# Performance work log

Measured on AMD Instinct MI355X. Metric: run time of the kernel, lower is better.

Reference implementation:

```python
import jax, jax.numpy as jnp
import numpy as np

S, B, V, E, H = 64, 32, 32000, 512, 1024


def gru_cell(x, h, Wih, Whh, bih, bhh):
    # PyTorch GRU cell math. x: [B, in], h: [B, H]
    gi = x @ Wih.T + bih          # [B, 3H]
    gh = h @ Whh.T + bhh          # [B, 3H]
    ir, iz, inn = jnp.split(gi, 3, axis=-1)
    hr, hz, hn = jnp.split(gh, 3, axis=-1)
    r = jax.nn.sigmoid(ir + hr)
    z = jax.nn.sigmoid(iz + hz)
    n = jnp.tanh(inn + r * hn)
    return (1.0 - z) * n + z * h


def run_gru(xs, h0, Wih, Whh, bih, bhh):
    def step(h, x):
        h = gru_cell(x, h, Wih, Whh, bih, bhh)
        return h, h
    _, hs = jax.lax.scan(step, h0, xs)
    return hs  # [S, B, H]


def setup_inputs():
    key = jax.random.key(0)
    ks = jax.random.split(key, 24)
    n = lambda k, shp, s=0.05: (jax.random.normal(k, shp, jnp.float32) * s)
    inp = {
        "input_seq": jax.random.randint(ks[0], (S, B), 0, V),
        "target_seq": jax.random.randint(ks[1], (S, B), 0, V),
        "emb": n(ks[2], (V, E)),
        # bidirectional encoder GRU (forward / backward directions)
        "enc_Wih_f": n(ks[3], (3 * H, E)), "enc_Whh_f": n(ks[4], (3 * H, H)),
        "enc_bih_f": n(ks[5], (3 * H,)),  "enc_bhh_f": n(ks[6], (3 * H,)),
        "enc_Wih_b": n(ks[7], (3 * H, E)), "enc_Whh_b": n(ks[8], (3 * H, H)),
        "enc_bih_b": n(ks[9], (3 * H,)),  "enc_bhh_b": n(ks[10], (3 * H,)),
        "encoder_init": n(ks[11], (2, H), 0.1),
        # decoder GRU: input = token(E) + glimpse(2H) + last_output(E)
        "dec_Wih": n(ks[12], (3 * H, 2 * E + 2 * H)), "dec_Whh": n(ks[13], (3 * H, H)),
        "dec_bih": n(ks[14], (3 * H,)), "dec_bhh": n(ks[15], (3 * H,)),
        "dec_init_h": n(ks[16], (H,), 0.1),
        "dec_init_out": n(ks[17], (E,), 0.1),
        "attn_W1": n(ks[18], (H, 3 * H)),  # Linear(3H -> H, bias=False)
        "attn_W2": n(ks[19], (1, H)),      # Linear(H -> 1, bias=False)
        "out_W": n(ks[20], (V, H)), "out_b": n(ks[21], (V,)),
    }
    return inp


def reference(input_seq, target_seq, emb,
              enc_Wih_f, enc_Whh_f, enc_bih_f, enc_bhh_f,
              enc_Wih_b, enc_Whh_b, enc_bih_b, enc_bhh_b, encoder_init,
              dec_Wih, dec_Whh, dec_bih, dec_bhh, dec_init_h, dec_init_out,
              attn_W1, attn_W2, out_W, out_b):
    x = emb[input_seq]            # [S, B, E]
    tgt = emb[target_seq]         # [S, B, E]
    bsz = x.shape[1]

    # bidirectional encoder
    h0f = jnp.broadcast_to(encoder_init[0], (bsz, H))
    h0b = jnp.broadcast_to(encoder_init[1], (bsz, H))
    fwd = run_gru(x, h0f, enc_Wih_f, enc_Whh_f, enc_bih_f, enc_bhh_f)
    bwd = run_gru(x[::-1], h0b, enc_Wih_b, enc_Whh_b, enc_bih_b, enc_bhh_b)[::-1]
    enc = jnp.concatenate([fwd, bwd], axis=-1)  # [S, B, 2H]

    def step(carry, inp_t):
        h, last_out = carry                      # [B,H], [B,E]
        tok, tg = inp_t                          # [B,E], [B,E]
        hexp = jnp.broadcast_to(h[None], (S, bsz, H))
        a = jnp.concatenate([enc, hexp], axis=-1)            # [S, B, 3H]
        scores = jnp.tanh(a @ attn_W1.T) @ attn_W2.T          # [S, B, 1]
        # NOTE: original uses nn.Softmax(dim=1) on [S,B,1] -> softmax over BATCH dim
        w = jax.nn.softmax(scores, axis=1)
        glimpse = (enc * w).sum(axis=0)                       # [B, 2H]
        dec_in = jnp.concatenate([tok, glimpse, last_out], axis=-1)
        h = gru_cell(dec_in, h, dec_Wih, dec_Whh, dec_bih, dec_bhh)
        probs = jax.nn.softmax(h @ out_W.T + out_b, axis=1)   # [B, V]
        return (h, tg), probs

    h0 = jnp.broadcast_to(dec_init_h, (bsz, H))
    o0 = jnp.broadcast_to(dec_init_out, (bsz, E))
    _, outs = jax.lax.scan(step, (h0, o0), (x, tgt))
    return outs  # [S, B, V]
```

## Files before the change

### kernel.cpp

```cpp
#include <hip/hip_runtime.h>
#include <hip/hip_bf16.h>

#define S_ 64
#define B_ 32
#define V_ 32000
#define E_ 512
#define H_ 1024
#define H3_ 3072

typedef __hip_bfloat16 bf16;
typedef __attribute__((ext_vector_type(8))) short s8v;
typedef __attribute__((ext_vector_type(4))) float f4;
typedef unsigned long long ull;

__device__ __forceinline__ float b2f(bf16 x){ return __bfloat162float(x); }
__device__ __forceinline__ bf16  f2b(float x){ return __float2bfloat16(x); }
__device__ __forceinline__ float bfu2f(unsigned short u){
  union { unsigned u; float f; } c; c.u = ((unsigned)u) << 16; return c.f;
}
#define MFMA16(a,b,c) __builtin_amdgcn_mfma_f32_16x16x32_bf16((a),(b),(c),0,0,0)

__device__ __forceinline__ float fsigmoid(float x){ return 1.f/(1.f + __expf(-x)); }
__device__ __forceinline__ float ftanh(float x){ float e2 = __expf(2.f*x); return 1.f - 2.f/(e2 + 1.f); }

__global__ __launch_bounds__(256) void cast_bf16_k(const float* __restrict__ s, bf16* __restrict__ d, int n8){
  int stride = gridDim.x*256;
  for (int i = blockIdx.x*256 + threadIdx.x; i < n8; i += stride){
    f4 a = *((const f4*)s + (size_t)i*2);
    f4 b = *((const f4*)s + (size_t)i*2 + 1);
    union { s8v v; bf16 h[8]; } o;
    #pragma unroll
    for (int k=0;k<4;k++){ o.h[k]=f2b(a[k]); o.h[4+k]=f2b(b[k]); }
    *((s8v*)d + i) = o.v;
  }
}
__global__ __launch_bounds__(256) void cast2_k(const float* __restrict__ s0, const float* __restrict__ s1,
                                               bf16* __restrict__ d0, bf16* __restrict__ d1, int n8){
  const float* s = blockIdx.y ? s1 : s0;
  bf16* d = blockIdx.y ? d1 : d0;
  int stride = gridDim.x*256;
  for (int i = blockIdx.x*256 + threadIdx.x; i < n8; i += stride){
    f4 a = *((const f4*)s + (size_t)i*2);
    f4 b = *((const f4*)s + (size_t)i*2 + 1);
    union { s8v v; bf16 h[8]; } o;
    #pragma unroll
    for (int k=0;k<4;k++){ o.h[k]=f2b(a[k]); o.h[4+k]=f2b(b[k]); }
    *((s8v*)d + i) = o.v;
  }
}
__global__ __launch_bounds__(256) void cast4_k(const float* __restrict__ s0, const float* __restrict__ s1,
                                               const float* __restrict__ s2, const float* __restrict__ s3,
                                               bf16* __restrict__ d0, bf16* __restrict__ d1,
                                               bf16* __restrict__ d2, bf16* __restrict__ d3, int n8){
  const float* s = (blockIdx.y==0)?s0:(blockIdx.y==1)?s1:(blockIdx.y==2)?s2:s3;
  bf16* d = (blockIdx.y==0)?d0:(blockIdx.y==1)?d1:(blockIdx.y==2)?d2:d3;
  int stride = gridDim.x*256;
  for (int i = blockIdx.x*256 + threadIdx.x; i < n8; i += stride){
    f4 a = *((const f4*)s + (size_t)i*2);
    f4 b = *((const f4*)s + (size_t)i*2 + 1);
    union { s8v v; bf16 h[8]; } o;
    #pragma unroll
    for (int k=0;k<4;k++){ o.h[k]=f2b(a[k]); o.h[4+k]=f2b(b[k]); }
    *((s8v*)d + i) = o.v;
  }
}
__global__ __launch_bounds__(256) void gather2_k(const float* __restrict__ emb,
                                                 const int* __restrict__ iseq, const int* __restrict__ tseq,
                                                 const float* __restrict__ o0,
                                                 bf16* __restrict__ dx, bf16* __restrict__ dlo){
  int i = blockIdx.x*256 + threadIdx.x;
  int row = i >> 6, e8 = i & 63;
  const float* src;
  bf16* d;
  if (blockIdx.y == 0){
    src = emb + (size_t)iseq[row]*E_;
    d = dx;
  } else {
    int t = row >> 5, b = row & 31;
    src = (t == 0) ? o0 : (emb + (size_t)tseq[(t-1)*B_ + b]*E_);
    d = dlo;
  }
  f4 a = *((const f4*)src + e8*2);
  f4 b = *((const f4*)src + e8*2 + 1);
  union { s8v v; bf16 h[8]; } o;
  #pragma unroll
  for (int k=0;k<4;k++){ o.h[k]=f2b(a[k]); o.h[4+k]=f2b(b[k]); }
  *((s8v*)d + i) = o.v;
}

template<int WB16, int ACC>
__global__ __launch_bounds__(256) void gemm_bt(const bf16* __restrict__ A, int lda,
                                               const bf16* __restrict__ B, int ldb,
                                               const float* __restrict__ bias,
                                               void* __restrict__ Cp, int ldc, int K)
{
  __shared__ bf16 a_sm[128][40];
  __shared__ bf16 b_sm[128][40];
  const int tid = threadIdx.x;
  const int m0 = blockIdx.y*128, n0 = blockIdx.x*128;
  const int w = tid>>6, l = tid&63;
  const int wm = w>>1, wn = w&1;
  f4 acc[4][4];
  #pragma unroll
  for (int i=0;i<4;i++)
    #pragma unroll
    for (int j=0;j<4;j++) acc[i][j] = (f4){0.f,0.f,0.f,0.f};
  const int srow = tid>>1, skc = (tid&1)*16;
  const int ar = l&15, koff = (l>>4)*8;
  for (int k0 = 0; k0 < K; k0 += 32){
    __syncthreads();
    const s8v* pa = (const s8v*)(A + (size_t)(m0+srow)*lda + k0 + skc);
    const s8v* pb = (const s8v*)(B + (size_t)(n0+srow)*ldb + k0 + skc);
    *(s8v*)&a_sm[srow][skc]   = pa[0];
    *(s8v*)&a_sm[srow][skc+8] = pa[1];
    *(s8v*)&b_sm[srow][skc]   = pb[0];
    *(s8v*)&b_sm[srow][skc+8] = pb[1];
    __syncthreads();
    s8v av[4], bv[4];
    #pragma unroll
    for (int i=0;i<4;i++) av[i] = *(const s8v*)&a_sm[wm*64 + i*16 + ar][koff];
    #pragma unroll
    for (int j=0;j<4;j++) bv[j] = *(const s8v*)&b_sm[wn*64 + j*16 + ar][koff];
    #pragma unroll
    for (int i=0;i<4;i++)
      #pragma unroll
      for (int j=0;j<4;j++)
        acc[i][j] = MFMA16(av[i], bv[j], acc[i][j]);
  }
  const int rb = (l>>4)*4;
  #pragma unroll
  for (int i=0;i<4;i++){
    #pragma unroll
    for (int j=0;j<4;j++){
      int col = n0 + wn*64 + j*16 + ar;
      float badd = bias ? bias[col] : 0.f;
      #pragma unroll
      for (int r=0;r<4;r++){
        int row = m0 + wm*64 + i*16 + rb + r;
        size_t idx = (size_t)row*ldc + col;
        float v = acc[i][j][r] + badd;
        if (ACC) v += ((const float*)Cp)[idx];
        if (WB16) ((bf16*)Cp)[idx] = f2b(v);
        else      ((float*)Cp)[idx] = v;
      }
    }
  }
}

__global__ __launch_bounds__(256) void out_gemm_k(
  const bf16* __restrict__ A, const bf16* __restrict__ Bw,
  const float* __restrict__ bias, bf16* __restrict__ C)
{
  __shared__ bf16 a_sm[128][40];
  __shared__ bf16 b_sm[128][40];
  const int tid = threadIdx.x;
  const int bid = blockIdx.x;
  const int xcd = bid & 7, kk = bid >> 3;
  const int super = kk >> 6, rem = kk & 63;
  const int sm = super & 1, sn = super >> 1;
  const int mi = rem & 7, nj = rem >> 3;
  const int mt = sm*8 + mi, nl = sn*8 + nj;
  const int nt = nl*8 + xcd;
  if (nt >= 250) return;
  const int m0 = mt*128, n0 = nt*128;
  const int w = tid>>6, l = tid&63;
  const int wm = w>>1, wn = w&1;
  f4 acc[4][4];
  #pragma unroll
  for (int i=0;i<4;i++)
    #pragma unroll
    for (int j=0;j<4;j++) acc[i][j] = (f4){0.f,0.f,0.f,0.f};
  const int srow = tid>>1, skc = (tid&1)*16;
  const int ar = l&15, koff = (l>>4)*8;
  for (int k0 = 0; k0 < 1024; k0 += 32){
    __syncthreads();
    const s8v* pa = (const s8v*)(A + (size_t)(m0+srow)*1024 + k0 + skc);
    const s8v* pb = (const s8v*)(Bw + (size_t)(n0+srow)*1024 + k0 + skc);
    *(s8v*)&a_sm[srow][skc]   = pa[0];
    *(s8v*)&a_sm[srow][skc+8] = pa[1];
    *(s8v*)&b_sm[srow][skc]   = pb[0];
    *(s8v*)&b_sm[srow][skc+8] = pb[1];
    __syncthreads();
    s8v av[4], bv[4];
    #pragma unroll
    for (int i=0;i<4;i++) av[i] = *(const s8v*)&a_sm[wm*64 + i*16 + ar][koff];
    #pragma unroll
    for (int j=0;j<4;j++) bv[j] = *(const s8v*)&b_sm[wn*64 + j*16 + ar][koff];
    #pragma unroll
    for (int i=0;i<4;i++)
      #pragma unroll
      for (int j=0;j<4;j++)
        acc[i][j] = MFMA16(av[i], bv[j], acc[i][j]);
  }
  const int rb = (l>>4)*4;
  float bj[4];
  #pragma unroll
  for (int j=0;j<4;j++) bj[j] = bias[n0 + wn*64 + j*16 + ar];
  #pragma unroll
  for (int i=0;i<4;i++){
    #pragma unroll
    for (int j=0;j<4;j++){
      const int col = n0 + wn*64 + j*16 + ar;
      #pragma unroll
      for (int r=0;r<4;r++){
        const int row = m0 + wm*64 + i*16 + rb + r;
        C[(size_t)row*V_ + col] = f2b(acc[i][j][r] + bj[j]);
      }
    }
  }
}

__global__ __launch_bounds__(256) void logit_stats_k(const bf16* __restrict__ lg,
                                                     float* __restrict__ rowM, float* __restrict__ rowL){
  __shared__ float wm[4], wl[4];
  const int tid = threadIdx.x;
  const bf16* p = lg + (size_t)blockIdx.x*V_;
  float m = -1e30f, lsum = 0.f;
  for (int c = tid; c < V_/8; c += 256){
    union { s8v v; unsigned short us[8]; } u;
    u.v = *((const s8v*)p + c);
    #pragma unroll
    for (int k = 0; k < 8; ++k){
      float v = bfu2f(u.us[k]);
      float mn = fmaxf(m, v);
      lsum = lsum*__expf(m - mn) + __expf(v - mn);
      m = mn;
    }
  }
  #pragma unroll
  for (int o = 32; o; o >>= 1){
    float mo = __shfl_xor(m, o), lo_ = __shfl_xor(lsum, o);
    float mn = fmaxf(m, mo);
    lsum = lsum*__expf(m - mn) + lo_*__expf(mo - mn);
    m = mn;
  }
  if ((tid&63)==0){ wm[tid>>6] = m; wl[tid>>6] = lsum; }
  __syncthreads();
  if (tid == 0){
    float M = fmaxf(fmaxf(wm[0],wm[1]), fmaxf(wm[2],wm[3]));
    float L = wl[0]*__expf(wm[0]-M) + wl[1]*__expf(wm[1]-M)
            + wl[2]*__expf(wm[2]-M) + wl[3]*__expf(wm[3]-M);
    rowM[blockIdx.x] = M;
    rowL[blockIdx.x] = L;
  }
}

__global__ __launch_bounds__(256) void norm_k(const bf16* __restrict__ lg,
                                              const float* __restrict__ rowM, const float* __restrict__ rowL,
                                              float* __restrict__ out){
  const int tid = threadIdx.x;
  const int row = blockIdx.x;
  const float M = rowM[row], inv = 1.f/rowL[row];
  const bf16* p = lg + (size_t)row*V_;
  float* q = out + (size_t)row*V_;
  for (int c = tid; c < V_/8; c += 256){
    union { s8v v; unsigned short us[8]; } u;
    u.v = *((const s8v*)p + c);
    f4 o0, o1;
    #pragma unroll
    for (int k = 0; k < 4; ++k) o0[k] = __expf(bfu2f(u.us[k]) - M)*inv;
    #pragma unroll
    for (int k = 0; k < 4; ++k) o1[k] = __expf(bfu2f(u.us[4+k]) - M)*inv;
    *((f4*)q + c*2)     = o0;
    *((f4*)q + c*2 + 1) = o1;
  }
}

__global__ __launch_bounds__(256) void enc_init_k(const float* __restrict__ enc_init,
                                                  const float* __restrict__ bihf, const float* __restrict__ bihb,
                                                  bf16* __restrict__ hb0, float* __restrict__ hfE,
                                                  float* __restrict__ bias_fb){
  int i = blockIdx.x*256 + threadIdx.x;
  int base = i*8;
  int dir = base>>15, rem = base&32767, col = rem&1023;
  const float* sp = enc_init + dir*H_ + col;
  f4 a = *(const f4*)sp, b = *(const f4*)(sp+4);
  union { s8v v; bf16 h[8]; } o;
  #pragma unroll
  for (int k=0;k<4;k++){ o.h[k]=f2b(a[k]); o.h[4+k]=f2b(b[k]); }
  *(s8v*)(hb0 + dir*32768 + rem) = o.v;
  *(f4*)(hfE + dir*32768 + rem) = a;
  *(f4*)(hfE + dir*32768 + rem + 4) = b;
  if (i < 6144) bias_fb[i] = (i < 3072) ? bihf[i] : bihb[i-3072];
}
__global__ __launch_bounds__(256) void dec_init_k(const float* __restrict__ dinh,
                                                  bf16* __restrict__ hd0, float* __restrict__ hfD){
  int i = blockIdx.x*256 + threadIdx.x;
  int base = i*8;
  int col = base&1023;
  const float* sp = dinh + col;
  f4 a = *(const f4*)sp, b = *(const f4*)(sp+4);
  union { s8v v; bf16 h[8]; } o;
  #pragma unroll
  for (int k=0;k<4;k++){ o.h[k]=f2b(a[k]); o.h[4+k]=f2b(b[k]); }
  *(s8v*)(hd0 + base) = o.v;
  *(f4*)(hfD + base) = a;
  *(f4*)(hfD + base + 4) = b;
}

__global__ __launch_bounds__(256) void enc_step_k(
  const float* __restrict__ gi_fb,
  const bf16* __restrict__ whhf, const bf16* __restrict__ whhb,
  const float* __restrict__ bhhf, const float* __restrict__ bhhb,
  const bf16* __restrict__ hrd_base, bf16* __restrict__ hwr_base,
  float* __restrict__ hfE, bf16* __restrict__ enc_out, int s)
{
  __shared__ bf16 hst[16][1032];
  __shared__ bf16 hsT[16][64];
  const int tid = threadIdx.x, bid = blockIdx.x;
  const int w = tid>>6, l = tid&63;
  const int lr = l&15, koff = (l>>4)*8, rb = (l>>4)*4;
  const int x = bid&7, g3 = bid>>3;
  const int dir = x>>2;
  const int mt = g3>>2;
  const int jtb = (x&3)*16 + (g3&3)*4;
  const int jt = jtb + w;
  const int col = jt*16 + lr;
  const bf16* W    = dir ? whhb : whhf;
  const float* bhh = dir ? bhhb : bhhf;
  const float br_ = bhh[col], bz_ = bhh[H_+col], bn_ = bhh[2*H_+col];
  const bf16* pr = W + (size_t)(jt*16 + lr)*H_ + koff;
  const bf16* pz = pr + (size_t)H_*H_;
  const bf16* pn = pz + (size_t)H_*H_;
  {
    const bf16* src = hrd_base + dir*32768 + (size_t)mt*16*H_;
    #pragma unroll
    for (int c = 0; c < 8; ++c){
      int g = c*256 + tid;
      int row = g>>7, off = g&127;
      *(s8v*)&hst[row][off*8] = *(const s8v*)(src + (size_t)row*H_ + off*8);
    }
  }
  __syncthreads();
  f4 accr = (f4){0,0,0,0}, accz = (f4){0,0,0,0}, accn = (f4){0,0,0,0};
  #pragma unroll 4
  for (int k0 = 0; k0 < H_; k0 += 32){
    s8v a = *(const s8v*)&hst[lr][koff + k0];
    accr = MFMA16(a, *(const s8v*)(pr + k0), accr);
    accz = MFMA16(a, *(const s8v*)(pz + k0), accz);
    accn = MFMA16(a, *(const s8v*)(pn + k0), accn);
  }
  const int es = dir ? (63 - s) : s;
  const int dcol = dir*3072 + col;
  #pragma unroll
  for (int ri = 0; ri < 4; ++ri){
    const int b_ = mt*16 + rb + ri;
    const size_t gr = (size_t)(es*B_ + b_)*6144;
    float ir = gi_fb[gr + dcol], iz = gi_fb[gr + 1024 + dcol], inn = gi_fb[gr + 2048 + dcol];
    float rg = fsigmoid(ir + accr[ri] + br_);
    float zg = fsigmoid(iz + accz[ri] + bz_);
    float ng = ftanh(inn + rg*(accn[ri] + bn_));
    float hold = hfE[dir*32768 + b_*H_ + col];
    float hnew = (1.f - zg)*ng + zg*hold;
    hfE[dir*32768 + b_*H_ + col] = hnew;
    hsT[rb+ri][w*16+lr] = f2b(hnew);
  }
  __syncthreads();
  {
    const int row = tid>>4, seg = tid&15;
    ull v = *(ull*)&hsT[row][seg*4];
    *(ull*)(hwr_base + dir*32768 + (size_t)(mt*16+row)*H_ + jtb*16 + seg*4) = v;
    *(ull*)(enc_out + (size_t)(es*B_ + mt*16+row)*2048 + dir*H_ + jtb*16 + seg*4) = v;
  }
}

__global__ __launch_bounds__(256) void dec_k1(
  const bf16* __restrict__ hd,
  const bf16* __restrict__ whhd, const float* __restrict__ bhhd,
  const bf16* __restrict__ w1b,
  float* __restrict__ gh, bf16* __restrict__ hW1b)
{
  __shared__ bf16 hst[16][1032];
  __shared__ float ghT[16][128];
  __shared__ bf16 hwT[16][128];
  const int tid = threadIdx.x, bid = blockIdx.x;
  const int w = tid>>6, l = tid&63;
  const int lr = l&15, koff = (l>>4)*8;
  const bool isP = bid < 16;
  const int hmt = isP ? (bid&1) : ((bid-16)&1);
  {
    const bf16* src = hd + (size_t)hmt*16*H_;
    #pragma unroll
    for (int c = 0; c < 8; ++c){
      int g = c*256 + tid;
      int row = g>>7, off = g&127;
      *(s8v*)&hst[row][off*8] = *(const s8v*)(src + (size_t)row*H_ + off*8);
    }
  }
  __syncthreads();
  if (isP){
    const int x2 = bid>>1;
    const int pjt0 = x2*8 + w*2;
    #pragma unroll
    for (int q = 0; q < 2; ++q){
      const bf16* pb = w1b + (size_t)((pjt0+q)*16 + lr)*H3_ + 2048 + koff;
      f4 acc = (f4){0,0,0,0};
      #pragma unroll 4
      for (int k0 = 0; k0 < H_; k0 += 32)
        acc = MFMA16(*(const s8v*)&hst[lr][koff+k0], *(const s8v*)(pb+k0), acc);
      #pragma unroll
      for (int r = 0; r < 4; ++r)
        hwT[(l>>4)*4+r][(w*2+q)*16 + lr] = f2b(acc[r]);
    }
    __syncthreads();
    #pragma unroll
    for (int i = 0; i < 2; ++i){
      int idx = tid + i*256;
      int row = idx>>5, seg = idx&31;
      *(ull*)(hW1b + (size_t)(hmt*16+row)*H_ + x2*128 + seg*4) = *(ull*)&hwT[row][seg*4];
    }
  } else {
    const int gb = bid - 16;
    const int rest = gb>>1;
    const int x3 = rest/3, gkk = rest%3;
    const int ntb = x3*24 + gkk*8;
    #pragma unroll
    for (int q = 0; q < 2; ++q){
      const int nt = ntb + w*2 + q;
      const bf16* pb = whhd + (size_t)(nt*16 + lr)*H_ + koff;
      const float bv = bhhd[nt*16 + lr];
      f4 acc = (f4){0,0,0,0};
      #pragma unroll 4
      for (int k0 = 0; k0 < H_; k0 += 32)
        acc = MFMA16(*(const s8v*)&hst[lr][koff+k0], *(const s8v*)(pb+k0), acc);
      #pragma unroll
      for (int r = 0; r < 4; ++r)
        ghT[(l>>4)*4+r][(w*2+q)*16 + lr] = acc[r] + bv;
    }
    __syncthreads();
    #pragma unroll
    for (int i = 0; i < 4; ++i){
      int idx = tid + i*256;
      int row = idx>>6, seg = idx&63;
      union{ float f[2]; ull u; } pk;
      pk.f[0] = ghT[row][seg*2]; pk.f[1] = ghT[row][seg*2+1];
      *(ull*)(gh + (size_t)(hmt*16+row)*H3_ + ntb*16 + seg*2) = pk.u;
    }
  }
}

__global__ __launch_bounds__(256) void dec_k2(
  const bf16* __restrict__ encW1b, const bf16* __restrict__ hW1b,
  const float* __restrict__ attnW2, float* __restrict__ wat)
{
  __shared__ float w2st[1024];
  __shared__ float scl[32];
  const int tid = threadIdx.x, s = blockIdx.x;
  w2st[tid] = attnW2[tid];
  w2st[tid+256] = attnW2[tid+256];
  w2st[tid+512] = attnW2[tid+512];
  w2st[tid+768] = attnW2[tid+768];
  __syncthreads();
  const int b = tid>>3, part = tid&7;
  const bf16* hp = hW1b + (size_t)b*H_ + part*128;
  const bf16* ep = encW1b + ((size_t)s*B_ + b)*H_ + part*128;
  const float* wp = w2st + part*128;
  float p = 0.f;
  #pragma unroll 4
  for (int ii = 0; ii < 16; ++ii){
    union { s8v v; unsigned short uu[8]; } hv, ev;
    hv.v = *(const s8v*)(hp + ii*8);
    ev.v = *(const s8v*)(ep + ii*8);
    #pragma unroll
    for (int k = 0; k < 8; ++k){
      float xx = bfu2f(ev.uu[k]) + bfu2f(hv.uu[k]);
      p += wp[ii*8+k]*ftanh(xx);
    }
  }
  p += __shfl_xor(p,1); p += __shfl_xor(p,2); p += __shfl_xor(p,4);
  if (part == 0) scl[b] = p;
  __syncthreads();
  if (tid < 32){
    float v = scl[tid];
    float m = v;
    #pragma unroll
    for (int o = 1; o <= 16; o <<= 1) m = fmaxf(m, __shfl_xor(m, o));
    float e = __expf(v - m);
    float Z = e;
    #pragma unroll
    for (int o = 1; o <= 16; o <<= 1) Z += __shfl_xor(Z, o);
    wat[s*B_ + tid] = e/Z;
  }
}

__global__ __launch_bounds__(256) void dec_k3(
  const float* __restrict__ gi_t,
  const bf16* __restrict__ encWgb, const float* __restrict__ gh,
  const float* __restrict__ wat,
  float* __restrict__ hfD, bf16* __restrict__ hd_w, bf16* __restrict__ hall_t)
{
  __shared__ float watst[64];
  __shared__ float part_[4][3][256];
  __shared__ bf16 hnewst[256];
  const int tid = threadIdx.x, bid = blockIdx.x;
  const int x = bid&7, g3 = bid>>3;
  const int db = 4*x + (g3&3), jq = g3>>2;
  const int jD = jq*256 + tid;
  if (tid < 64) watst[tid] = wat[tid*B_ + db];
  __syncthreads();
  const int lane = tid&63, wv = tid>>6;
  const int j0 = jq*256 + lane*4;
  f4 g0 = (f4){0,0,0,0}, g1 = (f4){0,0,0,0}, g2 = (f4){0,0,0,0};
  #pragma unroll 4
  for (int i = 0; i < 16; ++i){
    const int s2 = wv*16 + i;
    const float wt = watst[s2];
    const bf16* ro = encWgb + ((size_t)s2*B_ + db)*H3_;
    union{ ull u; unsigned short us[4]; } v0, v1, v2;
    v0.u = *(const ull*)(ro + j0);
    v1.u = *(const ull*)(ro + H_ + j0);
    v2.u = *(const ull*)(ro + 2*H_ + j0);
    #pragma unroll
    for (int k = 0; k < 4; ++k){
      g0[k] += wt*bfu2f(v0.us[k]);
      g1[k] += wt*bfu2f(v1.us[k]);
      g2[k] += wt*bfu2f(v2.us[k]);
    }
  }
  *(f4*)&part_[wv][0][lane*4] = g0;
  *(f4*)&part_[wv][1][lane*4] = g1;
  *(f4*)&part_[wv][2][lane*4] = g2;
  __syncthreads();
  float G0 = part_[0][0][tid]+part_[1][0][tid]+part_[2][0][tid]+part_[3][0][tid];
  float G1 = part_[0][1][tid]+part_[1][1][tid]+part_[2][1][tid]+part_[3][1][tid];
  float G2 = part_[0][2][tid]+part_[1][2][tid]+part_[2][2][tid]+part_[3][2][tid];
  const float* gp = gi_t + (size_t)db*H3_ + jD;
  float ir  = gp[0]    + G0;
  float iz  = gp[H_]   + G1;
  float inn = gp[2*H_] + G2;
  float hr_ = gh[(size_t)db*H3_ + jD];
  float hz_ = gh[(size_t)db*H3_ + H_ + jD];
  float hn_ = gh[(size_t)db*H3_ + 2*H_ + jD];
  float rg = fsigmoid(ir + hr_);
  float zg = fsigmoid(iz + hz_);
  float ng = ftanh(inn + rg*hn_);
  float hold = hfD[(size_t)db*H_ + jD];
  float hnew = (1.f - zg)*ng + zg*hold;
  hfD[(size_t)db*H_ + jD] = hnew;
  hnewst[tid] = f2b(hnew);
  __syncthreads();
  if (tid < 64){
    ull v = *(ull*)&hnewst[tid*4];
    *(ull*)(hd_w + (size_t)db*H_ + jq*256 + tid*4) = v;
    *(ull*)(hall_t + (size_t)db*H_ + jq*256 + tid*4) = v;
  }
}

extern "C" void kernel_launch(void* const* d_in, const int* in_sizes, int n_in,
                              void* d_out, int out_size, void* d_ws, size_t ws_size,
                              hipStream_t stream)
{
  (void)in_sizes; (void)n_in; (void)out_size; (void)ws_size;
  const int*   iseq  = (const int*)d_in[0];
  const int*   tseq  = (const int*)d_in[1];
  const float* emb   = (const float*)d_in[2];
  const float* wihf  = (const float*)d_in[3];
  const float* whhf_f= (const float*)d_in[4];
  const float* bihf  = (const float*)d_in[5];
  const float* bhhf  = (const float*)d_in[6];
  const float* wihb  = (const float*)d_in[7];
  const float* whhb_f= (const float*)d_in[8];
  const float* bihb  = (const float*)d_in[9];
  const float* bhhb  = (const float*)d_in[10];
  const float* einit = (const float*)d_in[11];
  const float* wihd  = (const float*)d_in[12];
  const float* whhd_f= (const float*)d_in[13];
  const float* bihd  = (const float*)d_in[14];
  const float* bhhd  = (const float*)d_in[15];
  const float* dinh  = (const float*)d_in[16];
  const float* dino  = (const float*)d_in[17];
  const float* w1    = (const float*)d_in[18];
  const float* w2    = (const float*)d_in[19];
  const float* outw  = (const float*)d_in[20];
  const float* outb  = (const float*)d_in[21];
  float* out = (float*)d_out;

  char* ws = (char*)d_ws;
  size_t off = 0;
  auto alloc = [&](size_t bytes)->char*{ char* p = ws + off; off += (bytes + 255) & ~(size_t)255; return p; };
  bf16* logits_b = (bf16*)ws;
  bf16* x_b      = (bf16*)alloc((size_t)2048*512*2);
  bf16* lo_b     = (bf16*)alloc((size_t)2048*512*2);
  bf16* wihf_b   = (bf16*)alloc((size_t)3072*512*2);
  bf16* wihb_b   = (bf16*)alloc((size_t)3072*512*2);
  bf16* whhf_b   = (bf16*)alloc((size_t)3072*1024*2);
  bf16* whhb_b   = (bf16*)alloc((size_t)3072*1024*2);
  bf16* wihd_b   = (bf16*)alloc((size_t)3072*3072*2);
  bf16* whhd_b   = (bf16*)alloc((size_t)3072*1024*2);
  bf16* w1_b     = (bf16*)alloc((size_t)1024*3072*2);
  float* gi_fb   = (float*)alloc((size_t)2048*6144*4);
  float* gi_d    = (float*)alloc((size_t)2048*3072*4);
  bf16* enc_b    = (bf16*)alloc((size_t)2048*2048*2);
  bf16* encW1_b  = (bf16*)alloc((size_t)2048*1024*2);
  bf16* encWg_b  = (bf16*)alloc((size_t)2048*3072*2);
  float* bias_fb = (float*)alloc((size_t)6144*4);
  bf16*  henc_b  = (bf16*)alloc((size_t)2*65536*2);
  float* hfE     = (float*)alloc((size_t)2*32768*4);
  bf16*  hdb     = (bf16*)alloc((size_t)2*32768*2);
  float* hfD     = (float*)alloc((size_t)32768*4);
  bf16*  hW1b    = (bf16*)alloc((size_t)32768*2);
  float* ghb     = (float*)alloc((size_t)32*3072*4);
  float* wat     = (float*)alloc((size_t)64*32*4);
  float* rowM    = (float*)alloc((size_t)2048*4);
  float* rowL    = (float*)alloc((size_t)2048*4);
  bf16* outw_b   = (bf16*)alloc((size_t)32000*1024*2);
  bf16*  hall_b  = (bf16*)alloc((size_t)2048*1024*2);

  gather2_k<<<dim3(512,2), 256, 0, stream>>>(emb, iseq, tseq, dino, x_b, lo_b);
  cast2_k<<<dim3(768,2),  256, 0, stream>>>(wihf, wihb, wihf_b, wihb_b, 196608);
  cast4_k<<<dim3(768,4),  256, 0, stream>>>(whhf_f, whhb_f, whhd_f, w1,
                                            whhf_b, whhb_b, whhd_b, w1_b, 393216);
  cast_bf16_k<<<2048, 256, 0, stream>>>(wihd, wihd_b, 1179648);
  cast_bf16_k<<<2048, 256, 0, stream>>>(outw, outw_b, 4096000);
  enc_init_k<<<32, 256, 0, stream>>>(einit, bihf, bihb, henc_b, hfE, bias_fb);

  gemm_bt<0,0><<<dim3(48,16), 256, 0, stream>>>(x_b, 512, wihf_b,      512,  bias_fb, gi_fb, 6144, 512);
  gemm_bt<0,0><<<dim3(24,16), 256, 0, stream>>>(x_b, 512, wihd_b,      3072, bihd,    gi_d,  3072, 512);
  gemm_bt<0,1><<<dim3(24,16), 256, 0, stream>>>(lo_b,512, wihd_b+2560, 3072, nullptr, gi_d,  3072, 512);

  for (int s = 0; s < 64; ++s){
    const bf16* hrd = henc_b + (size_t)(s&1)*65536;
    bf16*       hwr = henc_b + (size_t)((s+1)&1)*65536;
    enc_step_k<<<64, 256, 0, stream>>>(gi_fb, whhf_b, whhb_b, bhhf, bhhb,
                                       hrd, hwr, hfE, enc_b, s);
  }

  gemm_bt<1,0><<<dim3(8,16),  256, 0, stream>>>(enc_b, 2048, w1_b,       3072, nullptr, encW1_b, 1024, 2048);
  gemm_bt<1,0><<<dim3(24,16), 256, 0, stream>>>(enc_b, 2048, wihd_b+512, 3072, nullptr, encWg_b, 3072, 2048);

  dec_init_k<<<16, 256, 0, stream>>>(dinh, hdb, hfD);
  for (int t = 0; t < 64; ++t){
    const bf16* hdr = hdb + (size_t)(t&1)*32768;
    bf16*       hdw = hdb + (size_t)((t+1)&1)*32768;
    dec_k1<<<64, 256, 0, stream>>>(hdr, whhd_b, bhhd, w1_b, ghb, hW1b);
    dec_k2<<<64, 256, 0, stream>>>(encW1_b, hW1b, w2, wat);
    dec_k3<<<128, 256, 0, stream>>>(gi_d + (size_t)t*B_*H3_, encWg_b, ghb, wat,
                                    hfD, hdw, hall_b + (size_t)t*B_*H_);
  }

  out_gemm_k<<<4096, 256, 0, stream>>>(hall_b, outw_b, outb, logits_b);
  logit_stats_k<<<2048, 256, 0, stream>>>(logits_b, rowM, rowL);
  norm_k<<<2048, 256, 0, stream>>>(logits_b, rowM, rowL, out);
}
```

Measured before the change: 3.162 ms.

## Merge prep kernels, fuse decoder input GEMMs, use direct global-to-LDS loads

All weight casts, embedding gathers and state initialisations are folded into one multi-task prep kernel, which removes several launches. The two decoder input-projection GEMMs are merged into a single dual-A kernel, so the float accumulate read-modify-write pass goes away. The GEMM tiles now load through global_load_lds with an unpadded 32-column LDS layout, which may bring back LDS bank conflicts on the MFMA fragment reads. The prep kernel uses a fixed 512-block grid per task, so the large out_W cast loops more times per thread.

Result: faster. 3.083 ms (median of 2 runs) (-2.5%).

```diff
diff --git a/kernel.cpp b/kernel.cpp
--- a/kernel.cpp
+++ b/kernel.cpp
@@ -23,79 +23,108 @@
 __device__ __forceinline__ float fsigmoid(float x){ return 1.f/(1.f + __expf(-x)); }
 __device__ __forceinline__ float ftanh(float x){ float e2 = __expf(2.f*x); return 1.f - 2.f/(e2 + 1.f); }
 
-__global__ __launch_bounds__(256) void cast_bf16_k(const float* __restrict__ s, bf16* __restrict__ d, int n8){
-  int stride = gridDim.x*256;
-  for (int i = blockIdx.x*256 + threadIdx.x; i < n8; i += stride){
-    f4 a = *((const f4*)s + (size_t)i*2);
-    f4 b = *((const f4*)s + (size_t)i*2 + 1);
-    union { s8v v; bf16 h[8]; } o;
-    #pragma unroll
-    for (int k=0;k<4;k++){ o.h[k]=f2b(a[k]); o.h[4+k]=f2b(b[k]); }
-    *((s8v*)d + i) = o.v;
-  }
-}
-__global__ __launch_bounds__(256) void cast2_k(const float* __restrict__ s0, const float* __restrict__ s1,
-                                               bf16* __restrict__ d0, bf16* __restrict__ d1, int n8){
-  const float* s = blockIdx.y ? s1 : s0;
-  bf16* d = blockIdx.y ? d1 : d0;
-  int stride = gridDim.x*256;
-  for (int i = blockIdx.x*256 + threadIdx.x; i < n8; i += stride){
-    f4 a = *((const f4*)s + (size_t)i*2);
-    f4 b = *((const f4*)s + (size_t)i*2 + 1);
-    union { s8v v; bf16 h[8]; } o;
-    #pragma unroll
-    for (int k=0;k<4;k++){ o.h[k]=f2b(a[k]); o.h[4+k]=f2b(b[k]); }
-    *((s8v*)d + i) = o.v;
-  }
-}
-__global__ __launch_bounds__(256) void cast4_k(const float* __restrict__ s0, const float* __restrict__ s1,
-                                               const float* __restrict__ s2, const float* __restrict__ s3,
-                                               bf16* __restrict__ d0, bf16* __restrict__ d1,
-                                               bf16* __restrict__ d2, bf16* __restrict__ d3, int n8){
-  const float* s = (blockIdx.y==0)?s0:(blockIdx.y==1)?s1:(blockIdx.y==2)?s2:s3;
-  bf16* d = (blockIdx.y==0)?d0:(blockIdx.y==1)?d1:(blockIdx.y==2)?d2:d3;
-  int stride = gridDim.x*256;
-  for (int i = blockIdx.x*256 + threadIdx.x; i < n8; i += stride){
-    f4 a = *((const f4*)s + (size_t)i*2);
-    f4 b = *((const f4*)s + (size_t)i*2 + 1);
-    union { s8v v; bf16 h[8]; } o;
-    #pragma unroll
-    for (int k=0;k<4;k++){ o.h[k]=f2b(a[k]); o.h[4+k]=f2b(b[k]); }
-    *((s8v*)d + i) = o.v;
-  }
-}
-__global__ __launch_bounds__(256) void gather2_k(const float* __restrict__ emb,
-                                                 const int* __restrict__ iseq, const int* __restrict__ tseq,
-                                                 const float* __restrict__ o0,
-                                                 bf16* __restrict__ dx, bf16* __restrict__ dlo){
-  int i = blockIdx.x*256 + threadIdx.x;
-  int row = i >> 6, e8 = i & 63;
-  const float* src;
-  bf16* d;
-  if (blockIdx.y == 0){
-    src = emb + (size_t)iseq[row]*E_;
-    d = dx;
-  } else {
-    int t = row >> 5, b = row & 31;
-    src = (t == 0) ? o0 : (emb + (size_t)tseq[(t-1)*B_ + b]*E_);
-    d = dlo;
-  }
-  f4 a = *((const f4*)src + e8*2);
-  f4 b = *((const f4*)src + e8*2 + 1);
+__device__ __forceinline__ void gl16(const bf16* g, bf16* l){
+  __builtin_amdgcn_global_load_lds((const __attribute__((address_space(1))) void*)g,
+                                   (__attribute__((address_space(3))) void*)l, 16, 0, 0);
+}
+
+__device__ __forceinline__ void cast8(const float* __restrict__ s, bf16* __restrict__ d, int i){
+  f4 a = *((const f4*)s + (size_t)i*2);
+  f4 b = *((const f4*)s + (size_t)i*2 + 1);
   union { s8v v; bf16 h[8]; } o;
   #pragma unroll
   for (int k=0;k<4;k++){ o.h[k]=f2b(a[k]); o.h[4+k]=f2b(b[k]); }
   *((s8v*)d + i) = o.v;
 }
 
-template<int WB16, int ACC>
+__global__ __launch_bounds__(256) void prep_all_k(
+  const float* __restrict__ emb, const int* __restrict__ iseq, const int* __restrict__ tseq,
+  const float* __restrict__ dino,
+  const float* __restrict__ wihf, const float* __restrict__ wihb,
+  const float* __restrict__ whhf, const float* __restrict__ whhb,
+  const float* __restrict__ whhd, const float* __restrict__ w1,
+  const float* __restrict__ wihd, const float* __restrict__ outw,
+  const float* __restrict__ einit, const float* __restrict__ bihf,
+  const float* __restrict__ bihb, const float* __restrict__ dinh,
+  bf16* __restrict__ x_b, bf16* __restrict__ lo_b,
+  bf16* __restrict__ wihf_b, bf16* __restrict__ wihb_b,
+  bf16* __restrict__ whhf_b, bf16* __restrict__ whhb_b,
+  bf16* __restrict__ whhd_b, bf16* __restrict__ w1_b,
+  bf16* __restrict__ wihd_b, bf16* __restrict__ outw_b,
+  bf16* __restrict__ henc_b, float* __restrict__ hfE, float* __restrict__ bias_fb,
+  bf16* __restrict__ hdb, float* __restrict__ hfD)
+{
+  const int task = blockIdx.y;
+  const int stride = gridDim.x*256;
+  const int i00 = blockIdx.x*256 + threadIdx.x;
+  if (task < 8){
+    const float* s; bf16* d; int n8;
+    switch(task){
+      case 0: s=wihf; d=wihf_b; n8=196608; break;
+      case 1: s=wihb; d=wihb_b; n8=196608; break;
+      case 2: s=whhf; d=whhf_b; n8=393216; break;
+      case 3: s=whhb; d=whhb_b; n8=393216; break;
+      case 4: s=whhd; d=whhd_b; n8=393216; break;
+      case 5: s=w1;   d=w1_b;   n8=393216; break;
+      case 6: s=wihd; d=wihd_b; n8=1179648; break;
+      default: s=outw; d=outw_b; n8=4096000; break;
+    }
+    for (int i = i00; i < n8; i += stride) cast8(s, d, i);
+  } else if (task == 8 || task == 9){
+    for (int i = i00; i < 131072; i += stride){
+      int row = i>>6, e8 = i&63;
+      const float* src; bf16* d;
+      if (task == 8){ src = emb + (size_t)iseq[row]*E_; d = x_b; }
+      else {
+        int t = row>>5, b = row&31;
+        src = (t == 0) ? dino : (emb + (size_t)tseq[(t-1)*B_ + b]*E_);
+        d = lo_b;
+      }
+      f4 a = *((const f4*)src + e8*2);
+      f4 b = *((const f4*)src + e8*2 + 1);
+      union { s8v v; bf16 h[8]; } o;
+      #pragma unroll
+      for (int k=0;k<4;k++){ o.h[k]=f2b(a[k]); o.h[4+k]=f2b(b[k]); }
+      *((s8v*)d + i) = o.v;
+    }
+  } else if (task == 10){
+    for (int i = i00; i < 8192; i += stride){
+      int base = i*8;
+      int dir = base>>15, rem = base&32767, col = rem&1023;
+      const float* sp = einit + dir*H_ + col;
+      f4 a = *(const f4*)sp, b = *(const f4*)(sp+4);
+      union { s8v v; bf16 h[8]; } o;
+      #pragma unroll
+      for (int k=0;k<4;k++){ o.h[k]=f2b(a[k]); o.h[4+k]=f2b(b[k]); }
+      *(s8v*)(henc_b + dir*32768 + rem) = o.v;
+      *(f4*)(hfE + dir*32768 + rem) = a;
+      *(f4*)(hfE + dir*32768 + rem + 4) = b;
+      if (i < 6144) bias_fb[i] = (i < 3072) ? bihf[i] : bihb[i-3072];
+    }
+  } else {
+    for (int i = i00; i < 4096; i += stride){
+      int base = i*8;
+      int col = base&1023;
+      const float* sp = dinh + col;
+      f4 a = *(const f4*)sp, b = *(const f4*)(sp+4);
+      union { s8v v; bf16 h[8]; } o;
+      #pragma unroll
+      for (int k=0;k<4;k++){ o.h[k]=f2b(a[k]); o.h[4+k]=f2b(b[k]); }
+      *(s8v*)(hdb + base) = o.v;
+      *(f4*)(hfD + base) = a;
+      *(f4*)(hfD + base + 4) = b;
+    }
+  }
+}
+
+template<int WB16>
 __global__ __launch_bounds__(256) void gemm_bt(const bf16* __restrict__ A, int lda,
                                                const bf16* __restrict__ B, int ldb,
                                                const float* __restrict__ bias,
                                                void* __restrict__ Cp, int ldc, int K)
 {
-  __shared__ bf16 a_sm[128][40];
-  __shared__ bf16 b_sm[128][40];
+  __shared__ bf16 a_sm[128][32];
+  __shared__ bf16 b_sm[128][32];
   const int tid = threadIdx.x;
   const int m0 = blockIdx.y*128, n0 = blockIdx.x*128;
   const int w = tid>>6, l = tid&63;
@@ -105,16 +134,16 @@
   for (int i=0;i<4;i++)
     #pragma unroll
     for (int j=0;j<4;j++) acc[i][j] = (f4){0.f,0.f,0.f,0.f};
-  const int srow = tid>>1, skc = (tid&1)*16;
   const int ar = l&15, koff = (l>>4)*8;
+  const int glr = l>>2, gls = (l&3)*8;
   for (int k0 = 0; k0 < K; k0 += 32){
     __syncthreads();
-    const s8v* pa = (const s8v*)(A + (size_t)(m0+srow)*lda + k0 + skc);
-    const s8v* pb = (const s8v*)(B + (size_t)(n0+srow)*ldb + k0 + skc);
-    *(s8v*)&a_sm[srow][skc]   = pa[0];
-    *(s8v*)&a_sm[srow][skc+8] = pa[1];
-    *(s8v*)&b_sm[srow][skc]   = pb[0];
-    *(s8v*)&b_sm[srow][skc+8] = pb[1];
+    #pragma unroll
+    for (int o = 0; o < 2; ++o){
+      const int oo = w*2 + o;
+      gl16(A + (size_t)(m0 + oo*16 + glr)*lda + k0 + gls, &a_sm[oo*16][0]);
+      gl16(B + (size_t)(n0 + oo*16 + glr)*ldb + k0 + gls, &b_sm[oo*16][0]);
+    }
     __syncthreads();
     s8v av[4], bv[4];
     #pragma unroll
@@ -139,7 +168,6 @@
         int row = m0 + wm*64 + i*16 + rb + r;
         size_t idx = (size_t)row*ldc + col;
         float v = acc[i][j][r] + badd;
-        if (ACC) v += ((const float*)Cp)[idx];
         if (WB16) ((bf16*)Cp)[idx] = f2b(v);
         else      ((float*)Cp)[idx] = v;
       }
@@ -147,12 +175,70 @@
   }
 }
 
+__global__ __launch_bounds__(256) void gemm_dual(const bf16* __restrict__ A1, const bf16* __restrict__ A2,
+                                                 const bf16* __restrict__ Bw, const float* __restrict__ bias,
+                                                 float* __restrict__ C)
+{
+  __shared__ bf16 a_sm[128][32];
+  __shared__ bf16 b_sm[128][32];
+  const int tid = threadIdx.x;
+  const int m0 = blockIdx.y*128, n0 = blockIdx.x*128;
+  const int w = tid>>6, l = tid&63;
+  const int wm = w>>1, wn = w&1;
+  f4 acc[4][4];
+  #pragma unroll
+  for (int i=0;i<4;i++)
+    #pragma unroll
+    for (int j=0;j<4;j++) acc[i][j] = (f4){0.f,0.f,0.f,0.f};
+  const int ar = l&15, koff = (l>>4)*8;
+  const int glr = l>>2, gls = (l&3)*8;
+  #pragma unroll 1
+  for (int p = 0; p < 2; ++p){
+    const bf16* Ax = p ? A2 : A1;
+    const int cb = p ? 2560 : 0;
+    for (int k0 = 0; k0 < 512; k0 += 32){
+      __syncthreads();
+      #pragma unroll
+      for (int o = 0; o < 2; ++o){
+        const int oo = w*2 + o;
+        gl16(Ax + (size_t)(m0 + oo*16 + glr)*512 + k0 + gls, &a_sm[oo*16][0]);
+        gl16(Bw + (size_t)(n0 + oo*16 + glr)*3072 + cb + k0 + gls, &b_sm[oo*16][0]);
+      }
+      __syncthreads();
+      s8v av[4], bv[4];
+      #pragma unroll
+      for (int i=0;i<4;i++) av[i] = *(const s8v*)&a_sm[wm*64 + i*16 + ar][koff];
+      #pragma unroll
+      for (int j=0;j<4;j++) bv[j] = *(const s8v*)&b_sm[wn*64 + j*16 + ar][koff];
+      #pragma unroll
+      for (int i=0;i<4;i++)
+        #pragma unroll
+        for (int j=0;j<4;j++)
+          acc[i][j] = MFMA16(av[i], bv[j], acc[i][j]);
+    }
+  }
+  const int rb = (l>>4)*4;
+  #pragma unroll
+  for (int i=0;i<4;i++){
+    #pragma unroll
+    for (int j=0;j<4;j++){
+      int col = n0 + wn*64 + j*16 + ar;
+      float badd = bias[col];
+      #pragma unroll
+      for (int r=0;r<4;r++){
+        int row = m0 + wm*64 + i*16 + rb + r;
+        C[(size_t)row*H3_ + col] = acc[i][j][r] + badd;
+      }
+    }
+  }
+}
+
 __global__ __launch_bounds__(256) void out_gemm_k(
   const bf16* __restrict__ A, const bf16* __restrict__ Bw,
   const float* __restrict__ bias, bf16* __restrict__ C)
 {
-  __shared__ bf16 a_sm[128][40];
-  __shared__ bf16 b_sm[128][40];
+  __shared__ bf16 a_sm[128][32];
+  __shared__ bf16 b_sm[128][32];
   const int tid = threadIdx.x;
   const int bid = blockIdx.x;
   const int xcd = bid & 7, kk = bid >> 3;
@@ -170,16 +256,16 @@
   for (int i=0;i<4;i++)
     #pragma unroll
     for (int j=0;j<4;j++) acc[i][j] = (f4){0.f,0.f,0.f,0.f};
-  const int srow = tid>>1, skc = (tid&1)*16;
   const int ar = l&15, koff = (l>>4)*8;
+  const int glr = l>>2, gls = (l&3)*8;
   for (int k0 = 0; k0 < 1024; k0 += 32){
     __syncthreads();
-    const s8v* pa = (const s8v*)(A + (size_t)(m0+srow)*1024 + k0 + skc);
-    const s8v* pb = (const s8v*)(Bw + (size_t)(n0+srow)*1024 + k0 + skc);
-    *(s8v*)&a_sm[srow][skc]   = pa[0];
-    *(s8v*)&a_sm[srow][skc+8] = pa[1];
-    *(s8v*)&b_sm[srow][skc]   = pb[0];
-    *(s8v*)&b_sm[srow][skc+8] = pb[1];
+    #pragma unroll
+    for (int o = 0; o < 2; ++o){
+      const int oo = w*2 + o;
+      gl16(A + (size_t)(m0 + oo*16 + glr)*1024 + k0 + gls, &a_sm[oo*16][0]);
+      gl16(Bw + (size_t)(n0 + oo*16 + glr)*1024 + k0 + gls, &b_sm[oo*16][0]);
+    }
     __syncthreads();
     s8v av[4], bv[4];
     #pragma unroll
@@ -264,38 +350,6 @@
     *((f4*)q + c*2)     = o0;
     *((f4*)q + c*2 + 1) = o1;
   }
-}
-
-__global__ __launch_bounds__(256) void enc_init_k(const float* __restrict__ enc_init,
-                                                  const float* __restrict__ bihf, const float* __restrict__ bihb,
-                                                  bf16* __restrict__ hb0, float* __restrict__ hfE,
-                                                  float* __restrict__ bias_fb){
-  int i = blockIdx.x*256 + threadIdx.x;
-  int base = i*8;
-  int dir = base>>15, rem = base&32767, col = rem&1023;
-  const float* sp = enc_init + dir*H_ + col;
-  f4 a = *(const f4*)sp, b = *(const f4*)(sp+4);
-  union { s8v v; bf16 h[8]; } o;
-  #pragma unroll
-  for (int k=0;k<4;k++){ o.h[k]=f2b(a[k]); o.h[4+k]=f2b(b[k]); }
-  *(s8v*)(hb0 + dir*32768 + rem) = o.v;
-  *(f4*)(hfE + dir*32768 + rem) = a;
-  *(f4*)(hfE + dir*32768 + rem + 4) = b;
-  if (i < 6144) bias_fb[i] = (i < 3072) ? bihf[i] : bihb[i-3072];
-}
-__global__ __launch_bounds__(256) void dec_init_k(const float* __restrict__ dinh,
-                                                  bf16* __restrict__ hd0, float* __restrict__ hfD){
-  int i = blockIdx.x*256 + threadIdx.x;
-  int base = i*8;
-  int col = base&1023;
-  const float* sp = dinh + col;
-  f4 a = *(const f4*)sp, b = *(const f4*)(sp+4);
-  union { s8v v; bf16 h[8]; } o;
-  #pragma unroll
-  for (int k=0;k<4;k++){ o.h[k]=f2b(a[k]); o.h[4+k]=f2b(b[k]); }
-  *(s8v*)(hd0 + base) = o.v;
-  *(f4*)(hfD + base) = a;
-  *(f4*)(hfD + base + 4) = b;
 }
 
 __global__ __launch_bounds__(256) void enc_step_k(
@@ -606,17 +660,15 @@
   bf16* outw_b   = (bf16*)alloc((size_t)32000*1024*2);
   bf16*  hall_b  = (bf16*)alloc((size_t)2048*1024*2);
 
-  gather2_k<<<dim3(512,2), 256, 0, stream>>>(emb, iseq, tseq, dino, x_b, lo_b);
-  cast2_k<<<dim3(768,2),  256, 0, stream>>>(wihf, wihb, wihf_b, wihb_b, 196608);
-  cast4_k<<<dim3(768,4),  256, 0, stream>>>(whhf_f, whhb_f, whhd_f, w1,
-                                            whhf_b, whhb_b, whhd_b, w1_b, 393216);
-  cast_bf16_k<<<2048, 256, 0, stream>>>(wihd, wihd_b, 1179648);
-  cast_bf16_k<<<2048, 256, 0, stream>>>(outw, outw_b, 4096000);
-  enc_init_k<<<32, 256, 0, stream>>>(einit, bihf, bihb, henc_b, hfE, bias_fb);
-
-  gemm_bt<0,0><<<dim3(48,16), 256, 0, stream>>>(x_b, 512, wihf_b,      512,  bias_fb, gi_fb, 6144, 512);
-  gemm_bt<0,0><<<dim3(24,16), 256, 0, stream>>>(x_b, 512, wihd_b,      3072, bihd,    gi_d,  3072, 512);
-  gemm_bt<0,1><<<dim3(24,16), 256, 0, stream>>>(lo_b,512, wihd_b+2560, 3072, nullptr, gi_d,  3072, 512);
+  prep_all_k<<<dim3(512,12), 256, 0, stream>>>(
+      emb, iseq, tseq, dino,
+      wihf, wihb, whhf_f, whhb_f, whhd_f, w1, wihd, outw,
+      einit, bihf, bihb, dinh,
+      x_b, lo_b, wihf_b, wihb_b, whhf_b, whhb_b, whhd_b, w1_b, wihd_b, outw_b,
+      henc_b, hfE, bias_fb, hdb, hfD);
+
+  gemm_bt<0><<<dim3(48,16), 256, 0, stream>>>(x_b, 512, wihf_b, 512, bias_fb, gi_fb, 6144, 512);
+  gemm_dual<<<dim3(24,16), 256, 0, stream>>>(x_b, lo_b, wihd_b, bihd, gi_d);
 
   for (int s = 0; s < 64; ++s){
     const bf16* hrd = henc_b + (size_t)(s&1)*65536;
@@ -625,10 +677,9 @@
                                        hrd, hwr, hfE, enc_b, s);
   }
 
-  gemm_bt<1,0><<<dim3(8,16),  256, 0, stream>>>(enc_b, 2048, w1_b,       3072, nullptr, encW1_b, 1024, 2048);
-  gemm_bt<1,0><<<dim3(24,16), 256, 0, stream>>>(enc_b, 2048, wihd_b+512, 3072, nullptr, encWg_b, 3072, 2048);
-
-  dec_init_k<<<16, 256, 0, stream>>>(dinh, hdb, hfD);
+  gemm_bt<1><<<dim3(8,16),  256, 0, stream>>>(enc_b, 2048, w1_b,       3072, nullptr, encW1_b, 1024, 2048);
+  gemm_bt<1><<<dim3(24,16), 256, 0, stream>>>(enc_b, 2048, wihd_b+512, 3072, nullptr, encWg_b, 3072, 2048);
+
   for (int t = 0; t < 64; ++t){
     const bf16* hdr = hdb + (size_t)(t&1)*32768;
     bf16*       hdw = hdb + (size_t)((t+1)&1)*32768;
```
